# Kernel optimization log

Measured on AMD Instinct MI355X. Metric: run time of the kernel, lower is better.

## Reference

```python
import jax, jax.numpy as jnp
import numpy as np

B, N, D, L, H, DH, M, FF = 4, 2048, 512, 6, 8, 64, 266, 2048
EPS_LN = 1e-5
KERNEL_EPS = 1e-4


def fixed_pos_emb(n, dim):
    # performer_pytorch FixedPositionalEmbedding: cat(sin, cos) over half-dims
    inv_freq = 1.0 / (10000.0 ** (jnp.arange(0, dim, 2, dtype=jnp.float32) / dim))
    t = jnp.arange(n, dtype=jnp.float32)
    s = jnp.einsum('i,j->ij', t, inv_freq)  # [n, dim//2]
    return jnp.concatenate([jnp.sin(s), jnp.cos(s)], axis=-1)  # [n, dim]


def layer_norm(x, g, b):
    mu = x.mean(-1, keepdims=True)
    var = ((x - mu) ** 2).mean(-1, keepdims=True)
    return (x - mu) * jax.lax.rsqrt(var + EPS_LN) * g + b


def rotate_every_two(t):
    t1 = t[..., ::2]
    t2 = t[..., 1::2]
    return jnp.stack([-t2, t1], axis=-1).reshape(t.shape)


def apply_rotary(q, k, sinu):
    # sinu: [n, DH] = cat(sin_half, cos_half); repeat each value twice (interleaved)
    half = sinu.shape[-1] // 2
    sin = jnp.repeat(sinu[:, :half], 2, axis=-1)  # [n, DH]
    cos = jnp.repeat(sinu[:, half:], 2, axis=-1)
    q = q * cos + rotate_every_two(q) * sin
    k = k * cos + rotate_every_two(k) * sin
    return q, k


def softmax_kernel(data, proj, is_query):
    # data: [B,H,N,DH], proj: [M,DH]
    d = data.shape[-1]
    data_normalizer = d ** -0.25
    ratio = proj.shape[0] ** -0.5
    data_dash = jnp.einsum('bhnd,md->bhnm', data * data_normalizer, proj)
    diag = (data ** 2).sum(-1) * 0.5 * (data_normalizer ** 2)  # [B,H,N]
    if is_query:
        m = jnp.max(data_dash, axis=-1, keepdims=True)
    else:
        m = jnp.max(data_dash)
    return ratio * (jnp.exp(data_dash - diag[..., None] - m) + KERNEL_EPS)


def linear_attention(qf, kf, v):
    # qf/kf: [B,H,N,M], v: [B,H,N,DH]  (non-causal FAVOR+)
    k_sum = kf.sum(axis=-2)  # [B,H,M]
    d_inv = 1.0 / jnp.einsum('bhnm,bhm->bhn', qf, k_sum)
    context = jnp.einsum('bhnm,bhne->bhme', kf, v)  # [B,H,M,DH]
    return jnp.einsum('bhme,bhnm,bhn->bhne', context, qf, d_inv)


def setup_inputs() -> dict:
    key = jax.random.key(0)
    ks = jax.random.split(key, 8)
    std = 0.02
    inp = {
        'x': jax.random.normal(ks[0], (B, N, D), jnp.float32),
        'Wq': jax.random.normal(ks[1], (L, D, H * DH), jnp.float32) * std,
        'Wk': jax.random.normal(ks[2], (L, D, H * DH), jnp.float32) * std,
        'Wv': jax.random.normal(ks[3], (L, D, H * DH), jnp.float32) * std,
        'Wo': jax.random.normal(ks[4], (L, H * DH, D), jnp.float32) * std,
        'proj': jax.random.normal(ks[5], (L, M, DH), jnp.float32),
        'ln1_g': jnp.ones((L, D), jnp.float32),
        'ln1_b': jnp.zeros((L, D), jnp.float32),
        'W1': jax.random.normal(ks[6], (L, D, FF), jnp.float32) * std,
        'b1': jnp.zeros((L, FF), jnp.float32),
        'W2': jax.random.normal(ks[7], (L, FF, D), jnp.float32) * std,
        'b2': jnp.zeros((L, D), jnp.float32),
        'ln2_g': jnp.ones((L, D), jnp.float32),
        'ln2_b': jnp.zeros((L, D), jnp.float32),
        'lnf_g': jnp.ones((D,), jnp.float32),
        'lnf_b': jnp.zeros((D,), jnp.float32),
    }
    return inp


def reference(x, Wq, Wk, Wv, Wo, proj, ln1_g, ln1_b, W1, b1, W2, b2, ln2_g, ln2_b, lnf_g, lnf_b):
    n = x.shape[1]
    x = x + fixed_pos_emb(n, D)[None]          # additive sinusoidal emb
    sinu = fixed_pos_emb(n, DH)                 # per-head rotary table [n, DH]
    for i in range(L):
        # --- PreLayerNorm FAVOR+ self-attention ---
        h = layer_norm(x, ln1_g[i], ln1_b[i])
        q = jnp.einsum('bnd,de->bne', h, Wq[i]).reshape(B, n, H, DH).transpose(0, 2, 1, 3)
        k = jnp.einsum('bnd,de->bne', h, Wk[i]).reshape(B, n, H, DH).transpose(0, 2, 1, 3)
        v = jnp.einsum('bnd,de->bne', h, Wv[i]).reshape(B, n, H, DH).transpose(0, 2, 1, 3)
        q, k = apply_rotary(q, k, sinu)
        qf = softmax_kernel(q, proj[i], True)
        kf = softmax_kernel(k, proj[i], False)
        o = linear_attention(qf, kf, v)         # [B,H,n,DH]
        o = o.transpose(0, 2, 1, 3).reshape(B, n, H * DH)
        x = x + jnp.einsum('bne,ed->bnd', o, Wo[i])
        # --- PreLayerNorm FFN (GELU) ---
        h = layer_norm(x, ln2_g[i], ln2_b[i])
        h = jax.nn.gelu(jnp.einsum('bnd,df->bnf', h, W1[i]) + b1[i], approximate=False)
        x = x + jnp.einsum('bnf,fd->bnd', h, W2[i]) + b2[i]
    return layer_norm(x, lnf_g, lnf_b)
```

## Files before the change

### kernel.cpp

```cpp
#include <hip/hip_runtime.h>
#include <hip/hip_bf16.h>
#include <cstdint>

typedef float v4f __attribute__((ext_vector_type(4)));
typedef short v8s __attribute__((ext_vector_type(8)));
typedef unsigned short u16;

#define N_SEQ 2048
#define D_MODEL 512
#define N_LAYER 6
#define N_HEAD 8
#define D_HEAD 64
#define M_FEAT 266
#define M_PAD 288
#define M_ALLOC 384
#define FF_DIM 2048
#define BATCH 4
#define ROWS 8192
#define BHN 65536

__device__ __forceinline__ float b2f(u16 u) {
  return __uint_as_float(((uint32_t)u) << 16);
}
__device__ __forceinline__ u16 f2b(float f) {
  union { __hip_bfloat16 h; u16 u; } c;
  c.h = __float2bfloat16(f);
  return c.u;
}
__device__ __forceinline__ float wave_sum(float v) {
#pragma unroll
  for (int o = 1; o < 64; o <<= 1) v += __shfl_xor(v, o);
  return v;
}
__device__ __forceinline__ float wave_max(float v) {
#pragma unroll
  for (int o = 1; o < 64; o <<= 1) v = fmaxf(v, __shfl_xor(v, o));
  return v;
}

__device__ __forceinline__ float gelu_f(float x) {
  float ax = fabsf(x) * 0.70710678118f;
  float tt = __builtin_amdgcn_rcpf(fmaf(0.3275911f, ax, 1.0f));
  float poly = tt * fmaf(tt, fmaf(tt, fmaf(tt, fmaf(tt, 1.061405429f, -1.453152027f),
                                           1.421413741f), -0.284496736f), 0.254829592f);
  float er = 1.0f - poly * __expf(-ax * ax);
  er = copysignf(er, x);
  return 0.5f * x * (1.0f + er);
}

__device__ __forceinline__ void mfma_bf16(v4f& d, v8s a, v8s b) {
  asm volatile("v_mfma_f32_16x16x32_bf16 %0, %1, %2, %0" : "+v"(d) : "v"(a), "v"(b));
}

__device__ __forceinline__ void async16(const u16* g, u16* l) {
  __builtin_amdgcn_global_load_lds(
      (const __attribute__((address_space(1))) uint32_t*)g,
      (__attribute__((address_space(3))) uint32_t*)l, 16, 0, 0);
}

template <int EPI, int KSPLIT>
__global__ void __launch_bounds__(512, 4)
gemm4s(const u16* __restrict__ A, const u16* __restrict__ B,
       void* __restrict__ Cv, const float* __restrict__ bias,
       int K, int ldc)
{
  extern __shared__ u16 lds[];
  const int t = threadIdx.x;
  const int lane = t & 63;
  const int w = t >> 6;
  const int wm = w >> 2;
  const int wn = w & 3;
  const int tiM = blockIdx.x << 7, tiN = blockIdx.y << 8;
  const int ks = (KSPLIT > 1) ? blockIdx.z : 0;
  const int kchunk = K / KSPLIT;
  const int NT = kchunk >> 5;

  const int rr = lane & 15;
  const int kq = (lane >> 4) << 3;
  const int sw = ((rr >> 1) & 3) << 3;
  const int cr = kq ^ sw;

  const int srow = t >> 2;
  const int scol = (((t & 3) ^ ((srow >> 1) & 3)) << 3);
  const u16* Abase = A + (long long)(tiM + srow) * K + scol + (long long)ks * kchunk;
  const u16* Bbase = B + (long long)(tiN + srow) * K + scol + (long long)ks * kchunk;
  const long long r128 = 128LL * K;

  v4f acc[4][4] = {};

  auto stageA = [&](int s, int kt) {
    async16(Abase + (long long)kt * 32, &lds[s * 4096 + t * 8]);
  };
  auto stageB = [&](int s, int kt) {
    u16* d = &lds[16384 + s * 8192 + t * 8];
    async16(Bbase + (long long)kt * 32, d);
    async16(Bbase + (long long)kt * 32 + r128, d + 4096);
  };

  stageB(0, 0);
  stageA(0, 0);
  stageB(1, 1);
  stageA(1, 1);
  stageA(2, 2);
  asm volatile("s_waitcnt vmcnt(4)" ::: "memory");
  __builtin_amdgcn_s_barrier();

  for (int kt = 0; kt < NT; ++kt) {
    const int ab = (kt & 3) * 4096;
    const int bb = 16384 + (kt % 3) * 8192;
    if (kt + 2 < NT) stageB((kt + 2) % 3, kt + 2);
    if (kt + 3 < NT) stageA((kt + 3) & 3, kt + 3);
    v8s af[4], bf[4];
#pragma unroll
    for (int i = 0; i < 4; i++) {
      af[i] = *(const v8s*)&lds[ab + (wm * 64 + i * 16 + rr) * 32 + cr];
      bf[i] = *(const v8s*)&lds[bb + (wn * 64 + i * 16 + rr) * 32 + cr];
    }
    __builtin_amdgcn_s_setprio(1);
#pragma unroll
    for (int m = 0; m < 4; m++)
#pragma unroll
      for (int n = 0; n < 4; n++) mfma_bf16(acc[m][n], af[m], bf[n]);
    __builtin_amdgcn_s_setprio(0);
    if (kt + 1 < NT) {
      if (kt + 3 < NT)      asm volatile("s_waitcnt vmcnt(4)" ::: "memory");
      else if (kt + 2 < NT) asm volatile("s_waitcnt vmcnt(3)" ::: "memory");
      else                  asm volatile("s_waitcnt vmcnt(0)" ::: "memory");
      __builtin_amdgcn_s_barrier();
    }
  }

  __builtin_amdgcn_sched_barrier(0);
  asm volatile("s_nop 7\ns_nop 7\ns_nop 7");
  __builtin_amdgcn_sched_barrier(0);

  const int r4 = (lane >> 4) << 2;
  const int cc = lane & 15;
#pragma unroll
  for (int mf = 0; mf < 4; mf++)
#pragma unroll
    for (int nf = 0; nf < 4; nf++)
#pragma unroll
      for (int i = 0; i < 4; i++) {
        int row = tiM + wm * 64 + mf * 16 + r4 + i;
        int col = tiN + wn * 64 + nf * 16 + cc;
        float v = acc[mf][nf][i];
        if (EPI == 0) {
          ((u16*)Cv)[(long long)row * ldc + col] = f2b(v);
        } else if (EPI == 3) {
          ((u16*)Cv)[(long long)row * ldc + col] = f2b(gelu_f(v + bias[col]));
        } else {
          ((float*)Cv)[((long long)ks * ROWS + row) * ldc + col] = v;
        }
      }
}

template <bool LAST>
__global__ void ff2red_ln(const float* __restrict__ part, const float* __restrict__ bias,
                          float* __restrict__ x, const float* __restrict__ g,
                          const float* __restrict__ bvec, void* __restrict__ out)
{
  const int row = blockIdx.x * 4 + (threadIdx.x >> 6);
  const int lane = threadIdx.x & 63;
  const long long base = (long long)row * D_MODEL + lane * 8;
  v4f s0 = {}, s1 = {};
#pragma unroll
  for (int ks = 0; ks < 4; ks++) {
    const float* p = part + (long long)ks * (ROWS * 512LL) + base;
    s0 += *(const v4f*)p;
    s1 += *(const v4f*)(p + 4);
  }
  v4f b0 = *(const v4f*)(bias + lane * 8);
  v4f b1 = *(const v4f*)(bias + lane * 8 + 4);
  v4f x0 = *(const v4f*)(x + base) + s0 + b0;
  v4f x1 = *(const v4f*)(x + base + 4) + s1 + b1;
  if (!LAST) {
    *(v4f*)(x + base) = x0;
    *(v4f*)(x + base + 4) = x1;
  }
  float s = x0[0] + x0[1] + x0[2] + x0[3] + x1[0] + x1[1] + x1[2] + x1[3];
  float sq = x0[0]*x0[0] + x0[1]*x0[1] + x0[2]*x0[2] + x0[3]*x0[3]
           + x1[0]*x1[0] + x1[1]*x1[1] + x1[2]*x1[2] + x1[3]*x1[3];
  s = wave_sum(s);
  sq = wave_sum(sq);
  float mu = s * (1.0f / D_MODEL);
  float var = sq * (1.0f / D_MODEL) - mu * mu;
  float rstd = rsqrtf(var + 1e-5f);
  v4f g0 = *(const v4f*)(g + lane * 8), g1 = *(const v4f*)(g + lane * 8 + 4);
  v4f bb0 = *(const v4f*)(bvec + lane * 8), bb1 = *(const v4f*)(bvec + lane * 8 + 4);
  float y[8];
#pragma unroll
  for (int j = 0; j < 4; j++) y[j] = (x0[j] - mu) * rstd * g0[j] + bb0[j];
#pragma unroll
  for (int j = 0; j < 4; j++) y[4 + j] = (x1[j] - mu) * rstd * g1[j] + bb1[j];
  if (LAST) {
    float* op = (float*)out + base;
    v4f o0 = {y[0], y[1], y[2], y[3]}, o1 = {y[4], y[5], y[6], y[7]};
    *(v4f*)op = o0;
    *(v4f*)(op + 4) = o1;
  } else {
    u16* op = (u16*)out + base;
    alignas(16) u16 tmp[8];
#pragma unroll
    for (int j = 0; j < 8; j++) tmp[j] = f2b(y[j]);
    *(v8s*)op = *(v8s*)tmp;
  }
}

template <int EPI, int BN, int KSPLIT>
__global__ void __launch_bounds__(256, 4)
gemm2(const u16* __restrict__ A, const u16* __restrict__ B,
      void* __restrict__ Cv, const float* __restrict__ bias,
      int K, int ldc, long long sA, long long sB, long long sC,
      float scale, int Ncap, int Mcap, unsigned int* __restrict__ gmax)
{
  __shared__ u16 As[2][128 * 32];
  __shared__ u16 Bs[2][BN * 32];
  __shared__ float smax[4];
  const int zz = blockIdx.z;
  const int z = (KSPLIT > 1) ? zz / KSPLIT : zz;
  const int ks = (KSPLIT > 1) ? zz % KSPLIT : 0;
  const int kchunk = K / KSPLIT;
  const u16* Ag = A + (long long)z * sA + ks * kchunk;
  const u16* Bg = B + (long long)z * sB + ks * kchunk;
  const int t = threadIdx.x;
  const int lane = t & 63;
  const int w = t >> 6;
  constexpr int NF = BN / 32;
  const int wm = (w >> 1) << 6;
  const int wn = (w & 1) * (BN / 2);
  const int tiM = blockIdx.x << 7, tiN = blockIdx.y * BN;

  const int srow = t >> 2;
  const int scol = (t & 3) << 3;
  const u16* Ap = Ag + (long long)(tiM + srow) * K + scol;
  const u16* Bp = Bg + (long long)(tiN + srow) * K + scol;
  const long long rstride = 64LL * K;

  const int rr = lane & 15;
  const int kc = (lane >> 4) << 3;

  v4f acc[4][NF] = {};

  const int nk = kchunk >> 5;
  auto stage = [&](int buf, int k0) {
    async16(Ap + k0, &As[buf][t * 8]);
    async16(Ap + k0 + rstride, &As[buf][t * 8 + 2048]);
    async16(Bp + k0, &Bs[buf][t * 8]);
    if (BN == 128) async16(Bp + k0 + rstride, &Bs[buf][t * 8 + 2048]);
  };

  stage(0, 0);
  __syncthreads();
  int cur = 0;
  for (int kt = 0; kt < nk; ++kt) {
    if (kt + 1 < nk) stage(cur ^ 1, (kt + 1) << 5);
    v8s af[4], bf[NF];
#pragma unroll
    for (int i = 0; i < 4; i++) af[i] = *(const v8s*)&As[cur][(wm + rr + i * 16) * 32 + kc];
#pragma unroll
    for (int i = 0; i < NF; i++) bf[i] = *(const v8s*)&Bs[cur][(wn + rr + i * 16) * 32 + kc];
#pragma unroll
    for (int fm = 0; fm < 4; fm++)
#pragma unroll
      for (int fn = 0; fn < NF; fn++)
        mfma_bf16(acc[fm][fn], af[fm], bf[fn]);
    __syncthreads();
    cur ^= 1;
  }

  __builtin_amdgcn_sched_barrier(0);
  asm volatile("s_nop 7\ns_nop 7\ns_nop 7");
  __builtin_amdgcn_sched_barrier(0);

  const int r4 = (lane >> 4) << 2;
  const int cc = lane & 15;
  float lmax = -3e38f;
#pragma unroll
  for (int fm = 0; fm < 4; fm++)
#pragma unroll
    for (int fn = 0; fn < NF; fn++)
#pragma unroll
      for (int i = 0; i < 4; i++) {
        int row = tiM + wm + fm * 16 + r4 + i;
        int col = tiN + wn + fn * 16 + cc;
        float v = acc[fm][fn][i];
        if (EPI == 5) {
          if (row < Mcap && col < Ncap)
            ((float*)Cv)[((long long)zz * M_ALLOC + row) * 64 + col] = v;
        } else if (EPI == 7) {
          if (col < M_FEAT) lmax = fmaxf(lmax, v * scale);
        }
      }

  if (EPI == 7) {
    lmax = wave_max(lmax);
    if (lane == 0) smax[w] = lmax;
    __syncthreads();
    if (t == 0) {
      float m = fmaxf(fmaxf(smax[0], smax[1]), fmaxf(smax[2], smax[3]));
      unsigned int u = __float_as_uint(m);
      unsigned int key = (u & 0x80000000u) ? ~u : (u | 0x80000000u);
      atomicMax(gmax, key);
    }
  }
}

__global__ void __launch_bounds__(384, 3)
kf_gemm(const u16* __restrict__ kr, const u16* __restrict__ proj,
        const float* __restrict__ diagk, const unsigned int* __restrict__ kmax,
        u16* __restrict__ kfT, float* __restrict__ part)
{
  __shared__ u16 As[2][288 * 32];
  __shared__ u16 Bs[2][64 * 32];
  __shared__ float sdg[64];
  const int ntile = blockIdx.x;
  const int bh = blockIdx.z;
  const int n0 = ntile << 6;
  const int t = threadIdx.x;
  const int lane = t & 63;
  const int w = t >> 6;
  const u16* Bg = kr + (long long)bh * (N_SEQ * 64) + (long long)n0 * 64;
  const int rr = lane & 15, kc = (lane >> 4) << 3;

  if (t < 64) sdg[t] = diagk[(long long)bh * N_SEQ + n0 + t];
  unsigned int kk = kmax[0];
  const float km = (kk & 0x80000000u) ? __uint_as_float(kk ^ 0x80000000u)
                                      : __uint_as_float(~kk);

  v4f acc[3][4] = {};
  auto stage = [&](int buf, int k0) {
#pragma unroll
    for (int j = 0; j < 3; j++) {
      int idx = j * 384 + t;
      async16(proj + (long long)(idx >> 2) * 64 + ((idx & 3) << 3) + k0,
              &As[buf][j * 3072 + t * 8]);
    }
    if (t < 256) async16(Bg + (long long)(t >> 2) * 64 + ((t & 3) << 3) + k0,
                         &Bs[buf][t * 8]);
  };

  stage(0, 0);
  __syncthreads();
  for (int kt = 0; kt < 2; ++kt) {
    if (kt == 0) stage(1, 32);
    v8s af[3], bf[4];
#pragma unroll
    for (int i = 0; i < 3; i++) af[i] = *(const v8s*)&As[kt][(w * 48 + i * 16 + rr) * 32 + kc];
#pragma unroll
    for (int i = 0; i < 4; i++) bf[i] = *(const v8s*)&Bs[kt][(i * 16 + rr) * 32 + kc];
#pragma unroll
    for (int fm = 0; fm < 3; fm++)
#pragma unroll
      for (int fn = 0; fn < 4; fn++)
        mfma_bf16(acc[fm][fn], af[fm], bf[fn]);
    __syncthreads();
  }

  __builtin_amdgcn_sched_barrier(0);
  asm volatile("s_nop 7\ns_nop 7\ns_nop 7");
  __builtin_amdgcn_sched_barrier(0);

  const int r4 = (lane >> 4) << 2;
  const int cc = lane & 15;
  const float sc = 0.35355339f;

#pragma unroll
  for (int fm = 0; fm < 3; fm++)
#pragma unroll
    for (int i = 0; i < 4; i++) {
      int m = w * 48 + fm * 16 + r4 + i;
      float s = 0.0f;
#pragma unroll
      for (int fn = 0; fn < 4; fn++) {
        float dd = acc[fm][fn][i] * sc;
        float kf = (m < M_FEAT)
            ? 0.06131389f * (__expf(dd - sdg[fn * 16 + cc] - km) + 1e-4f) : 0.0f;
        acc[fm][fn][i] = kf;
        s += kf;
        kfT[((long long)bh * M_ALLOC + m) * N_SEQ + n0 + fn * 16 + cc] = f2b(kf);
      }
#pragma unroll
      for (int o = 1; o < 16; o <<= 1) s += __shfl_xor(s, o);
      if (cc == 0) part[((long long)bh * M_PAD + m) * 32 + ntile] = s;
    }
}

__global__ void ksumred(const float* __restrict__ part, float* __restrict__ ksum)
{
  int i = blockIdx.x * 256 + threadIdx.x;
  if (i >= 32 * M_PAD) return;
  const float* p = part + (long long)i * 32;
  float s = 0.0f;
#pragma unroll
  for (int j = 0; j < 32; j += 4) {
    v4f v = *(const v4f*)(p + j);
    s += v[0] + v[1] + v[2] + v[3];
  }
  ksum[i] = s;
}

template <int EPI>
__global__ void __launch_bounds__(256, 6)
gemm_small(const u16* __restrict__ A, const u16* __restrict__ B,
           void* __restrict__ Cv, const float* __restrict__ bias,
           int K, int ldc, long long sA, long long sB)
{
  __shared__ u16 As[2][64 * 32];
  __shared__ u16 Bs[2][64 * 32];
  const int z = blockIdx.z;
  const u16* Ag = A + (long long)z * sA;
  const u16* Bg = B + (long long)z * sB;
  const int t = threadIdx.x;
  const int lane = t & 63;
  const int w = t >> 6;
  const int wm = (w >> 1) << 5;
  const int wn = (w & 1) << 5;
  const int tiM = blockIdx.x << 6, tiN = blockIdx.y << 6;

  const int srow = t >> 2;
  const int scol = (t & 3) << 3;
  const u16* Ap = Ag + (long long)(tiM + srow) * K + scol;
  const u16* Bp = Bg + (long long)(tiN + srow) * K + scol;

  const int rr = lane & 15;
  const int kc = (lane >> 4) << 3;

  v4f acc[2][2] = {};

  const int nk = K >> 5;
  auto stage = [&](int buf, int k0) {
    async16(Ap + k0, &As[buf][t * 8]);
    async16(Bp + k0, &Bs[buf][t * 8]);
  };

  stage(0, 0);
  __syncthreads();
  int cur = 0;
  for (int kt = 0; kt < nk; ++kt) {
    if (kt + 1 < nk) stage(cur ^ 1, (kt + 1) << 5);
    v8s af[2], bf[2];
#pragma unroll
    for (int i = 0; i < 2; i++) af[i] = *(const v8s*)&As[cur][(wm + rr + i * 16) * 32 + kc];
#pragma unroll
    for (int i = 0; i < 2; i++) bf[i] = *(const v8s*)&Bs[cur][(wn + rr + i * 16) * 32 + kc];
#pragma unroll
    for (int fm = 0; fm < 2; fm++)
#pragma unroll
      for (int fn = 0; fn < 2; fn++)
        mfma_bf16(acc[fm][fn], af[fm], bf[fn]);
    __syncthreads();
    cur ^= 1;
  }

  __builtin_amdgcn_sched_barrier(0);
  asm volatile("s_nop 7\ns_nop 7\ns_nop 7");
  __builtin_amdgcn_sched_barrier(0);

  const int r4 = (lane >> 4) << 2;
  const int cc = lane & 15;
#pragma unroll
  for (int fm = 0; fm < 2; fm++)
#pragma unroll
    for (int fn = 0; fn < 2; fn++)
#pragma unroll
      for (int i = 0; i < 4; i++) {
        int row = tiM + wm + fm * 16 + r4 + i;
        int col = tiN + wn + fn * 16 + cc;
        float v = acc[fm][fn][i];
        if (EPI == 2) {
          long long idx = (long long)row * ldc + col;
          float bb = bias ? bias[col] : 0.0f;
          ((float*)Cv)[idx] += v + bb;
        } else {
          int b_ = z >> 3, h_ = z & 7;
          ((u16*)Cv)[(long long)(b_ * N_SEQ + row) * 512 + h_ * 64 + col] = f2b(v);
        }
      }
}

__global__ void __launch_bounds__(384, 3)
ddq_qf(const u16* __restrict__ qr, const u16* __restrict__ proj,
       const float* __restrict__ diag, const float* __restrict__ ksum,
       u16* __restrict__ qf)
{
  __shared__ u16 As[2][64 * 32];
  __shared__ u16 Bs[2][288 * 32];
  __shared__ float redw[6][64];
  __shared__ float rowv[64];
  __shared__ float sdg[64];
  const int bh = blockIdx.z;
  const int tiM = blockIdx.x << 6;
  const int t = threadIdx.x;
  const int lane = t & 63;
  const int w = t >> 6;
  const u16* Ag = qr + (long long)bh * (N_SEQ * 64);
  const int srow = t >> 2, scol = (t & 3) << 3;
  const u16* Ap = Ag + (long long)(tiM + srow) * 64 + scol;
  const int rr = lane & 15, kc = (lane >> 4) << 3;
  const int wn = w * 48;

  if (t < 64) sdg[t] = diag[(long long)bh * N_SEQ + tiM + t];

  v4f acc[4][3] = {};
  auto stage = [&](int buf, int k0) {
    if (t < 256) async16(Ap + k0, &As[buf][t * 8]);
#pragma unroll
    for (int j = 0; j < 3; j++) {
      int idx = j * 384 + t;
      async16(proj + (long long)(idx >> 2) * 64 + ((idx & 3) << 3) + k0,
              &Bs[buf][j * 3072 + t * 8]);
    }
  };

  stage(0, 0);
  __syncthreads();
  for (int kt = 0; kt < 2; ++kt) {
    if (kt == 0) stage(1, 32);
    v8s af[4], bf[3];
#pragma unroll
    for (int i = 0; i < 4; i++) af[i] = *(const v8s*)&As[kt][(rr + i * 16) * 32 + kc];
#pragma unroll
    for (int i = 0; i < 3; i++) bf[i] = *(const v8s*)&Bs[kt][(wn + i * 16 + rr) * 32 + kc];
#pragma unroll
    for (int fm = 0; fm < 4; fm++)
#pragma unroll
      for (int fn = 0; fn < 3; fn++)
        mfma_bf16(acc[fm][fn], af[fm], bf[fn]);
    __syncthreads();
  }

  __builtin_amdgcn_sched_barrier(0);
  asm volatile("s_nop 7\ns_nop 7\ns_nop 7");
  __builtin_amdgcn_sched_barrier(0);

  const int r4 = (lane >> 4) << 2;
  const int cc = lane & 15;
  const float sc = 0.35355339f;

#pragma unroll
  for (int fm = 0; fm < 4; fm++)
#pragma unroll
    for (int i = 0; i < 4; i++) {
      float m = -3e38f;
#pragma unroll
      for (int fn = 0; fn < 3; fn++) {
        int col = wn + fn * 16 + cc;
        float v = acc[fm][fn][i] * sc;
        if (col < M_FEAT) m = fmaxf(m, v);
      }
#pragma unroll
      for (int o = 1; o < 16; o <<= 1) m = fmaxf(m, __shfl_xor(m, o));
      if (cc == 0) redw[w][fm * 16 + r4 + i] = m;
    }
  __syncthreads();
  if (t < 64) {
    float g = redw[0][t];
#pragma unroll
    for (int ww = 1; ww < 6; ww++) g = fmaxf(g, redw[ww][t]);
    rowv[t] = g;
  }
  __syncthreads();

  float ksv[3];
#pragma unroll
  for (int fn = 0; fn < 3; fn++) ksv[fn] = ksum[bh * M_PAD + wn + fn * 16 + cc];

#pragma unroll
  for (int fm = 0; fm < 4; fm++)
#pragma unroll
    for (int i = 0; i < 4; i++) {
      int row = fm * 16 + r4 + i;
      float gm = rowv[row];
      float dg = sdg[row];
      float s = 0.0f;
#pragma unroll
      for (int fn = 0; fn < 3; fn++) {
        float e = 0.06131389f * (__expf(acc[fm][fn][i] * sc - dg - gm) + 1e-4f);
        acc[fm][fn][i] = e;
        s += e * ksv[fn];
      }
#pragma unroll
      for (int o = 1; o < 16; o <<= 1) s += __shfl_xor(s, o);
      if (cc == 0) redw[w][row] = s;
    }
  __syncthreads();
  if (t < 64) {
    float s = redw[0][t];
#pragma unroll
    for (int ww = 1; ww < 6; ww++) s += redw[ww][t];
    rowv[t] = 1.0f / s;
  }
  __syncthreads();

#pragma unroll
  for (int fm = 0; fm < 4; fm++)
#pragma unroll
    for (int i = 0; i < 4; i++) {
      int row = fm * 16 + r4 + i;
      float dinv = rowv[row];
#pragma unroll
      for (int fn = 0; fn < 3; fn++) {
        int col = wn + fn * 16 + cc;
        qf[((long long)bh * N_SEQ + tiM + row) * M_PAD + col] =
            f2b(acc[fm][fn][i] * dinv);
      }
    }
}

template <bool F32OUT>
__global__ void ln_kernel(const float* __restrict__ x, const float* __restrict__ g,
                          const float* __restrict__ b, void* __restrict__ out)
{
  const int row = blockIdx.x * 4 + (threadIdx.x >> 6);
  const int lane = threadIdx.x & 63;
  const float* xr = x + (long long)row * D_MODEL + lane * 8;
  v4f v0 = *(const v4f*)xr;
  v4f v1 = *(const v4f*)(xr + 4);
  float s = v0[0] + v0[1] + v0[2] + v0[3] + v1[0] + v1[1] + v1[2] + v1[3];
  float sq = v0[0]*v0[0] + v0[1]*v0[1] + v0[2]*v0[2] + v0[3]*v0[3]
           + v1[0]*v1[0] + v1[1]*v1[1] + v1[2]*v1[2] + v1[3]*v1[3];
  s = wave_sum(s);
  sq = wave_sum(sq);
  float mu = s * (1.0f / D_MODEL);
  float var = sq * (1.0f / D_MODEL) - mu * mu;
  float rstd = rsqrtf(var + 1e-5f);
  v4f g0 = *(const v4f*)(g + lane * 8), g1 = *(const v4f*)(g + lane * 8 + 4);
  v4f bb0 = *(const v4f*)(b + lane * 8), bb1 = *(const v4f*)(b + lane * 8 + 4);
  float y[8];
#pragma unroll
  for (int j = 0; j < 4; j++) y[j] = (v0[j] - mu) * rstd * g0[j] + bb0[j];
#pragma unroll
  for (int j = 0; j < 4; j++) y[4 + j] = (v1[j] - mu) * rstd * g1[j] + bb1[j];
  if (F32OUT) {
    float* op = (float*)out + (long long)row * D_MODEL + lane * 8;
    v4f o0 = {y[0], y[1], y[2], y[3]}, o1 = {y[4], y[5], y[6], y[7]};
    *(v4f*)op = o0;
    *(v4f*)(op + 4) = o1;
  } else {
    u16* op = (u16*)out + (long long)row * D_MODEL + lane * 8;
    alignas(16) u16 tmp[8];
#pragma unroll
    for (int j = 0; j < 8; j++) tmp[j] = f2b(y[j]);
    *(v8s*)op = *(v8s*)tmp;
  }
}

__global__ void posadd(const float* __restrict__ xin, float* __restrict__ x)
{
  long long i = (long long)blockIdx.x * 256 + threadIdx.x;
  int d = (int)(i & 511);
  int n = (int)((i >> 9) & 2047);
  int j = d & 255;
  float sarg = (float)n * expf(-0.035977892f * (float)j);
  float pe = (d < 256) ? sinf(sarg) : cosf(sarg);
  x[i] = xin[i] + pe;
}

__global__ void rotab(float* __restrict__ ts, float* __restrict__ tc)
{
  int i = blockIdx.x * 64 + threadIdx.x;
  int n = i >> 5, j = i & 31;
  float sarg = (float)n * expf(-0.28782314f * (float)j);
  float s, c;
  sincosf(sarg, &s, &c);
  ts[i] = s;
  tc[i] = c;
}

__global__ void __launch_bounds__(256)
rotvt(const u16* __restrict__ qkv,
      const float* __restrict__ ts, const float* __restrict__ tc,
      u16* __restrict__ qr, u16* __restrict__ kr, u16* __restrict__ vT,
      float* __restrict__ dq, float* __restrict__ dk)
{
  __shared__ u16 st[64][72];
  const int bid = blockIdx.x;
  const int nt = bid & 31;
  const int h = (bid >> 5) & 7;
  const int b = bid >> 8;
  const int t = threadIdx.x;
  const int r = t >> 3;
  const int cg = t & 7;
#pragma unroll
  for (int it = 0; it < 2; ++it) {
    const int nl = it * 32 + r;
    const int n = nt * 64 + nl;
    const long long src = ((long long)(b * N_SEQ + n)) * 1536 + h * 64 + cg * 8;
    v8s q8 = *(const v8s*)(qkv + src);
    v8s k8 = *(const v8s*)(qkv + src + 512);
    v8s v8 = *(const v8s*)(qkv + src + 1024);
    v4f sn = *(const v4f*)(ts + n * 32 + cg * 4);
    v4f cn = *(const v4f*)(tc + n * 32 + cg * 4);
    alignas(16) u16 qo[8], ko[8];
    float q2 = 0.0f, k2 = 0.0f;
#pragma unroll
    for (int j = 0; j < 4; j++) {
      float qe = b2f((u16)q8[2 * j]), qoe = b2f((u16)q8[2 * j + 1]);
      float ke = b2f((u16)k8[2 * j]), koe = b2f((u16)k8[2 * j + 1]);
      float c = cn[j], s = sn[j];
      float q0 = qe * c - qoe * s, q1 = qoe * c + qe * s;
      float k0 = ke * c - koe * s, k1 = koe * c + ke * s;
      qo[2 * j] = f2b(q0); qo[2 * j + 1] = f2b(q1);
      ko[2 * j] = f2b(k0); ko[2 * j + 1] = f2b(k1);
      q2 += q0 * q0 + q1 * q1;
      k2 += k0 * k0 + k1 * k1;
    }
    q2 += __shfl_xor(q2, 1); q2 += __shfl_xor(q2, 2); q2 += __shfl_xor(q2, 4);
    k2 += __shfl_xor(k2, 1); k2 += __shfl_xor(k2, 2); k2 += __shfl_xor(k2, 4);
    const long long rowidx = (long long)(b * 8 + h) * N_SEQ + n;
    if (cg == 0) {
      dq[rowidx] = q2 * 0.0625f;
      dk[rowidx] = k2 * 0.0625f;
    }
    *(v8s*)(qr + rowidx * 64 + cg * 8) = *(v8s*)qo;
    *(v8s*)(kr + rowidx * 64 + cg * 8) = *(v8s*)ko;
    *(v8s*)&st[nl][cg * 8] = v8;
  }
  __syncthreads();
  const int r2 = t >> 2, c2 = (t & 3) << 4;
  alignas(16) u16 tmp[16];
#pragma unroll
  for (int jj = 0; jj < 16; jj++) tmp[jj] = st[c2 + jj][r2];
  const long long dst = ((long long)((b * 8 + h) * 64 + r2)) * N_SEQ + nt * 64 + c2;
  *(v8s*)(vT + dst) = *(v8s*)&tmp[0];
  *(v8s*)(vT + dst + 8) = *(v8s*)&tmp[8];
}

__global__ void wtrans(const float* __restrict__ src, u16* __restrict__ dst,
                       int Ks, int Ns, long long sSrc, long long sDst)
{
  int l = blockIdx.z;
  src += (long long)l * sSrc;
  dst += (long long)l * sDst;
  int n0 = blockIdx.x << 6, k0 = blockIdx.y << 6;
  __shared__ float st[64][68];
  int t = threadIdx.x;
  int r = t >> 2, c = (t & 3) << 4;
  const float* sp = src + (long long)(k0 + r) * Ns + n0 + c;
#pragma unroll
  for (int jj = 0; jj < 16; jj += 4) *(v4f*)&st[r][c + jj] = *(const v4f*)(sp + jj);
  __syncthreads();
  alignas(16) u16 tmp[16];
#pragma unroll
  for (int jj = 0; jj < 16; jj++) tmp[jj] = f2b(st[c + jj][r]);
  u16* dp = dst + (long long)(n0 + r) * Ks + k0 + c;
  *(v8s*)(dp) = *(v8s*)&tmp[0];
  *(v8s*)(dp + 8) = *(v8s*)&tmp[8];
}

__global__ void projconv(const float* __restrict__ proj, u16* __restrict__ out)
{
  int i = blockIdx.x * 256 + threadIdx.x;
  int dh = i & 63;
  int m = (i >> 6) % M_ALLOC;
  int l = i / (M_ALLOC * 64);
  float v = (m < M_FEAT) ? proj[((long long)l * M_FEAT + m) * 64 + dh] : 0.0f;
  out[i] = f2b(v);
}

__global__ void resetmax(unsigned int* p) { *p = 0u; }

__global__ void ctxred(const float* __restrict__ part, u16* __restrict__ ctxT)
{
  int bh = blockIdx.y;
  int m0 = blockIdx.x << 6;
  __shared__ float st[64][65];
  int t = threadIdx.x;
  int r = t >> 2, c = (t & 3) << 4;
  int m = m0 + r;
  v4f s[4] = {};
  if (m < M_PAD) {
    for (int ks = 0; ks < 8; ks++) {
      const float* p = part + (((long long)bh * 8 + ks) * M_ALLOC + m) * 64 + c;
#pragma unroll
      for (int j = 0; j < 4; j++) s[j] += *(const v4f*)(p + j * 4);
    }
  }
#pragma unroll
  for (int j = 0; j < 4; j++)
#pragma unroll
    for (int e = 0; e < 4; e++) st[r][c + j * 4 + e] = s[j][e];
  __syncthreads();
  int e = t >> 2, mc = (t & 3) << 4;
  if (m0 + mc < M_PAD) {
    alignas(16) u16 tmp[16];
#pragma unroll
    for (int j = 0; j < 16; j++) tmp[j] = f2b(st[mc + j][e]);
    u16* op = ctxT + ((long long)bh * 64 + e) * M_PAD + m0 + mc;
    *(v8s*)op = *(v8s*)&tmp[0];
    *(v8s*)(op + 8) = *(v8s*)&tmp[8];
  }
}

extern "C" void kernel_launch(void* const* d_in, const int* in_sizes, int n_in,
                              void* d_out, int out_size, void* d_ws, size_t ws_size,
                              hipStream_t stream)
{
  const float* x_in = (const float*)d_in[0];
  const float* Wq  = (const float*)d_in[1];
  const float* Wk  = (const float*)d_in[2];
  const float* Wv  = (const float*)d_in[3];
  const float* Wo  = (const float*)d_in[4];
  const float* Pr  = (const float*)d_in[5];
  const float* ln1g = (const float*)d_in[6];
  const float* ln1b = (const float*)d_in[7];
  const float* W1  = (const float*)d_in[8];
  const float* b1  = (const float*)d_in[9];
  const float* W2  = (const float*)d_in[10];
  const float* b2  = (const float*)d_in[11];
  const float* ln2g = (const float*)d_in[12];
  const float* ln2b = (const float*)d_in[13];
  const float* lnfg = (const float*)d_in[14];
  const float* lnfb = (const float*)d_in[15];

  hipFuncSetAttribute(reinterpret_cast<const void*>(&gemm4s<0, 1>),
                      hipFuncAttributeMaxDynamicSharedMemorySize, 81920);
  hipFuncSetAttribute(reinterpret_cast<const void*>(&gemm4s<3, 1>),
                      hipFuncAttributeMaxDynamicSharedMemorySize, 81920);
  hipFuncSetAttribute(reinterpret_cast<const void*>(&gemm4s<5, 4>),
                      hipFuncAttributeMaxDynamicSharedMemorySize, 81920);

  char* ws = (char*)d_ws;
  size_t off = 0;
  auto alloc = [&](size_t bytes) -> void* {
    void* p = ws + off;
    off = (off + bytes + 255) & ~(size_t)255;
    return p;
  };

  float* x      = (float*)alloc((size_t)ROWS * D_MODEL * 4);
  float* tsin   = (float*)alloc((size_t)N_SEQ * 32 * 4);
  float* tcos   = (float*)alloc((size_t)N_SEQ * 32 * 4);
  u16*   wqkvT  = (u16*)alloc((size_t)N_LAYER * 1536 * 512 * 2);
  u16*   woT    = (u16*)alloc((size_t)N_LAYER * 512 * 512 * 2);
  u16*   w1T    = (u16*)alloc((size_t)N_LAYER * 2048 * 512 * 2);
  u16*   w2T    = (u16*)alloc((size_t)N_LAYER * 512 * 2048 * 2);
  u16*   projT  = (u16*)alloc((size_t)N_LAYER * M_ALLOC * 64 * 2);
  u16*   hbuf   = (u16*)alloc((size_t)ROWS * D_MODEL * 2);
  u16*   obuf   = (u16*)alloc((size_t)ROWS * D_MODEL * 2);
  float* big    = (float*)alloc((size_t)32 * N_SEQ * M_PAD * 4);
  u16*   qrbuf  = (u16*)alloc((size_t)BHN * 64 * 2);
  u16*   krbuf  = (u16*)alloc((size_t)BHN * 64 * 2);
  u16*   vTbuf  = (u16*)alloc((size_t)BHN * 64 * 2);
  float* diagq  = (float*)alloc((size_t)BHN * 4);
  float* diagk  = (float*)alloc((size_t)BHN * 4);
  unsigned int* kmaxu = (unsigned int*)alloc(256);
  u16*   kfT    = (u16*)alloc((size_t)32 * M_ALLOC * N_SEQ * 2);
  float* part   = (float*)alloc((size_t)32 * 8 * M_ALLOC * 64 * 4);
  float* kspart = (float*)alloc((size_t)32 * M_PAD * 32 * 4);
  u16*   ctxT   = (u16*)alloc((size_t)32 * 64 * M_PAD * 2);
  float* ksum   = (float*)alloc((size_t)32 * M_PAD * 4);
  (void)alloc(1 << 20);
  (void)ws_size; (void)in_sizes; (void)n_in; (void)out_size;
  float* ff2part = (float*)kfT;

  posadd<<<16384, 256, 0, stream>>>(x_in, x);
  rotab<<<1024, 64, 0, stream>>>(tsin, tcos);
  wtrans<<<dim3(8, 8, 6), 256, 0, stream>>>(Wq, wqkvT, 512, 512, 512LL * 512, 1536LL * 512);
  wtrans<<<dim3(8, 8, 6), 256, 0, stream>>>(Wk, wqkvT + 512LL * 512, 512, 512, 512LL * 512, 1536LL * 512);
  wtrans<<<dim3(8, 8, 6), 256, 0, stream>>>(Wv, wqkvT + 1024LL * 512, 512, 512, 512LL * 512, 1536LL * 512);
  wtrans<<<dim3(8, 8, 6), 256, 0, stream>>>(Wo, woT, 512, 512, 512LL * 512, 512LL * 512);
  wtrans<<<dim3(32, 8, 6), 256, 0, stream>>>(W1, w1T, 512, 2048, 512LL * 2048, 2048LL * 512);
  wtrans<<<dim3(8, 32, 6), 256, 0, stream>>>(W2, w2T, 2048, 512, 2048LL * 512, 512LL * 2048);
  projconv<<<(N_LAYER * M_ALLOC * 64) / 256, 256, 0, stream>>>(Pr, projT);

  ln_kernel<false><<<ROWS / 4, 256, 0, stream>>>(x, ln1g, ln1b, hbuf);

  for (int l = 0; l < N_LAYER; l++) {
    const u16* wq = wqkvT + (long long)l * 1536 * 512;
    const u16* wo = woT + (long long)l * 512 * 512;
    const u16* w1 = w1T + (long long)l * 2048 * 512;
    const u16* w2 = w2T + (long long)l * 512 * 2048;
    const u16* pj = projT + (long long)l * M_ALLOC * 64;

    resetmax<<<1, 1, 0, stream>>>(kmaxu);
    gemm4s<0, 1><<<dim3(64, 6), 512, 81920, stream>>>(hbuf, wq, big, nullptr, 512, 1536);
    rotvt<<<1024, 256, 0, stream>>>((u16*)big, tsin, tcos, qrbuf, krbuf, vTbuf, diagq, diagk);
    gemm2<7, 128, 1><<<dim3(512, 3, 1), 256, 0, stream>>>(krbuf, pj, nullptr, nullptr,
        64, M_PAD, 0, 0, 0, 0.35355339f, M_PAD, BHN, kmaxu);
    kf_gemm<<<dim3(32, 1, 32), 384, 0, stream>>>(krbuf, pj, diagk, kmaxu, kfT, kspart);
    ksumred<<<(32 * M_PAD + 255) / 256, 256, 0, stream>>>(kspart, ksum);
    gemm2<5, 64, 8><<<dim3(3, 1, 256), 256, 0, stream>>>(kfT, vTbuf, part, nullptr,
        2048, 64, (long long)M_ALLOC * N_SEQ, 64LL * N_SEQ, 0, 1.0f, 64, M_PAD, nullptr);
    ctxred<<<dim3(5, 32), 256, 0, stream>>>(part, ctxT);
    ddq_qf<<<dim3(32, 1, 32), 384, 0, stream>>>(qrbuf, pj, diagq, ksum, kfT);
    gemm_small<4><<<dim3(32, 1, 32), 256, 0, stream>>>(kfT, ctxT, obuf, nullptr,
        M_PAD, 0, (long long)N_SEQ * M_PAD, 64LL * M_PAD);
    gemm_small<2><<<dim3(128, 8, 1), 256, 0, stream>>>(obuf, wo, x, nullptr,
        512, 512, 0, 0);
    ln_kernel<false><<<ROWS / 4, 256, 0, stream>>>(x, ln2g + l * 512, ln2b + l * 512, hbuf);
    gemm4s<3, 1><<<dim3(64, 8), 512, 81920, stream>>>(hbuf, w1, big, b1 + (long long)l * 2048,
        512, 2048);
    gemm4s<5, 4><<<dim3(64, 2, 4), 512, 81920, stream>>>((u16*)big, w2, ff2part, nullptr,
        2048, 512);
    if (l < N_LAYER - 1) {
      ff2red_ln<false><<<2048, 256, 0, stream>>>(ff2part, b2 + (long long)l * 512, x,
          ln1g + (long long)(l + 1) * 512, ln1b + (long long)(l + 1) * 512, hbuf);
    } else {
      ff2red_ln<true><<<2048, 256, 0, stream>>>(ff2part, b2 + (long long)l * 512, x,
          lnfg, lnfb, d_out);
    }
  }
}
```

Baseline: 1.406 ms.

## Fuse query feature map with context GEMM to produce attention output directly

The qf kernel now keeps the normalized query features in shared memory and multiplies them by the per-head context matrix in the same block. The output rows go straight to obuf, so the separate gemm_small<4> launch is gone, along with the round trip of the full qf tensor through global memory. The cost is 75 KB of dynamic LDS per block, which may lower occupancy, and only 4 of the 6 waves do the second GEMM. Unused template branches in gemm_small and ln_kernel are removed as cleanup.

```diff
diff --git a/kernel.cpp b/kernel.cpp
--- a/kernel.cpp
+++ b/kernel.cpp
@@ -468,24 +468,18 @@
         int row = tiM + wm + fm * 16 + r4 + i;
         int col = tiN + wn + fn * 16 + cc;
         float v = acc[fm][fn][i];
-        if (EPI == 2) {
-          long long idx = (long long)row * ldc + col;
-          float bb = bias ? bias[col] : 0.0f;
-          ((float*)Cv)[idx] += v + bb;
-        } else {
-          int b_ = z >> 3, h_ = z & 7;
-          ((u16*)Cv)[(long long)(b_ * N_SEQ + row) * 512 + h_ * 64 + col] = f2b(v);
-        }
+        long long idx = (long long)row * ldc + col;
+        float bb = bias ? bias[col] : 0.0f;
+        ((float*)Cv)[idx] += v + bb;
       }
 }
 
 __global__ void __launch_bounds__(384, 3)
-ddq_qf(const u16* __restrict__ qr, const u16* __restrict__ proj,
-       const float* __restrict__ diag, const float* __restrict__ ksum,
-       u16* __restrict__ qf)
-{
-  __shared__ u16 As[2][64 * 32];
-  __shared__ u16 Bs[2][288 * 32];
+ddq_qf_o(const u16* __restrict__ qr, const u16* __restrict__ proj,
+         const float* __restrict__ diag, const float* __restrict__ ksum,
+         const u16* __restrict__ ctxT, u16* __restrict__ obuf)
+{
+  extern __shared__ u16 dl[];
   __shared__ float redw[6][64];
   __shared__ float rowv[64];
   __shared__ float sdg[64];
@@ -495,8 +489,7 @@
   const int lane = t & 63;
   const int w = t >> 6;
   const u16* Ag = qr + (long long)bh * (N_SEQ * 64);
-  const int srow = t >> 2, scol = (t & 3) << 3;
-  const u16* Ap = Ag + (long long)(tiM + srow) * 64 + scol;
+  const u16* Ap = Ag + (long long)(tiM + (t >> 2)) * 64 + ((t & 3) << 3);
   const int rr = lane & 15, kc = (lane >> 4) << 3;
   const int wn = w * 48;
 
@@ -504,12 +497,12 @@
 
   v4f acc[4][3] = {};
   auto stage = [&](int buf, int k0) {
-    if (t < 256) async16(Ap + k0, &As[buf][t * 8]);
+    if (t < 256) async16(Ap + k0, &dl[buf * 2048 + t * 8]);
 #pragma unroll
     for (int j = 0; j < 3; j++) {
       int idx = j * 384 + t;
       async16(proj + (long long)(idx >> 2) * 64 + ((idx & 3) << 3) + k0,
-              &Bs[buf][j * 3072 + t * 8]);
+              &dl[4096 + buf * 9216 + j * 3072 + t * 8]);
     }
   };
 
@@ -519,9 +512,11 @@
     if (kt == 0) stage(1, 32);
     v8s af[4], bf[3];
 #pragma unroll
-    for (int i = 0; i < 4; i++) af[i] = *(const v8s*)&As[kt][(rr + i * 16) * 32 + kc];
-#pragma unroll
-    for (int i = 0; i < 3; i++) bf[i] = *(const v8s*)&Bs[kt][(wn + i * 16 + rr) * 32 + kc];
+    for (int i = 0; i < 4; i++)
+      af[i] = *(const v8s*)&dl[kt * 2048 + (rr + i * 16) * 32 + kc];
+#pragma unroll
+    for (int i = 0; i < 3; i++)
+      bf[i] = *(const v8s*)&dl[4096 + kt * 9216 + (wn + i * 16 + rr) * 32 + kc];
 #pragma unroll
     for (int fm = 0; fm < 4; fm++)
 #pragma unroll
@@ -533,6 +528,14 @@
   __builtin_amdgcn_sched_barrier(0);
   asm volatile("s_nop 7\ns_nop 7\ns_nop 7");
   __builtin_amdgcn_sched_barrier(0);
+
+  v8s creg[6];
+  const u16* cb = ctxT + (long long)bh * (64 * M_PAD);
+#pragma unroll
+  for (int j = 0; j < 6; j++) {
+    int slot = j * 384 + t;
+    creg[j] = *(const v8s*)(cb + (slot / 36) * M_PAD + (slot % 36) * 8);
+  }
 
   const int r4 = (lane >> 4) << 2;
   const int cc = lane & 15;
@@ -600,15 +603,41 @@
       int row = fm * 16 + r4 + i;
       float dinv = rowv[row];
 #pragma unroll
-      for (int fn = 0; fn < 3; fn++) {
-        int col = wn + fn * 16 + cc;
-        qf[((long long)bh * N_SEQ + tiM + row) * M_PAD + col] =
-            f2b(acc[fm][fn][i] * dinv);
+      for (int fn = 0; fn < 3; fn++)
+        dl[row * 296 + wn + fn * 16 + cc] = f2b(acc[fm][fn][i] * dinv);
+    }
+#pragma unroll
+  for (int j = 0; j < 6; j++) {
+    int slot = j * 384 + t;
+    *(v8s*)&dl[18944 + (slot / 36) * 296 + (slot % 36) * 8] = creg[j];
+  }
+  __syncthreads();
+
+  if (w < 4) {
+    v4f oacc[4] = {};
+    for (int kk = 0; kk < 9; kk++) {
+      v8s aq = *(const v8s*)&dl[(w * 16 + rr) * 296 + kk * 32 + kc];
+#pragma unroll
+      for (int et = 0; et < 4; et++) {
+        v8s bc = *(const v8s*)&dl[18944 + (et * 16 + rr) * 296 + kk * 32 + kc];
+        mfma_bf16(oacc[et], aq, bc);
       }
     }
-}
-
-template <bool F32OUT>
+    __builtin_amdgcn_sched_barrier(0);
+    asm volatile("s_nop 7\ns_nop 7\ns_nop 7");
+    __builtin_amdgcn_sched_barrier(0);
+    const int b_ = bh >> 3, h_ = bh & 7;
+#pragma unroll
+    for (int et = 0; et < 4; et++)
+#pragma unroll
+      for (int i = 0; i < 4; i++) {
+        int n = tiM + w * 16 + r4 + i;
+        obuf[((long long)(b_ * N_SEQ + n)) * 512 + h_ * 64 + et * 16 + cc] =
+            f2b(oacc[et][i]);
+      }
+  }
+}
+
 __global__ void ln_kernel(const float* __restrict__ x, const float* __restrict__ g,
                           const float* __restrict__ b, void* __restrict__ out)
 {
@@ -632,18 +661,11 @@
   for (int j = 0; j < 4; j++) y[j] = (v0[j] - mu) * rstd * g0[j] + bb0[j];
 #pragma unroll
   for (int j = 0; j < 4; j++) y[4 + j] = (v1[j] - mu) * rstd * g1[j] + bb1[j];
-  if (F32OUT) {
-    float* op = (float*)out + (long long)row * D_MODEL + lane * 8;
-    v4f o0 = {y[0], y[1], y[2], y[3]}, o1 = {y[4], y[5], y[6], y[7]};
-    *(v4f*)op = o0;
-    *(v4f*)(op + 4) = o1;
-  } else {
-    u16* op = (u16*)out + (long long)row * D_MODEL + lane * 8;
-    alignas(16) u16 tmp[8];
-#pragma unroll
-    for (int j = 0; j < 8; j++) tmp[j] = f2b(y[j]);
-    *(v8s*)op = *(v8s*)tmp;
-  }
+  u16* op = (u16*)out + (long long)row * D_MODEL + lane * 8;
+  alignas(16) u16 tmp[8];
+#pragma unroll
+  for (int j = 0; j < 8; j++) tmp[j] = f2b(y[j]);
+  *(v8s*)op = *(v8s*)tmp;
 }
 
 __global__ void posadd(const float* __restrict__ xin, float* __restrict__ x)
@@ -820,6 +842,8 @@
                       hipFuncAttributeMaxDynamicSharedMemorySize, 81920);
   hipFuncSetAttribute(reinterpret_cast<const void*>(&gemm4s<5, 4>),
                       hipFuncAttributeMaxDynamicSharedMemorySize, 81920);
+  hipFuncSetAttribute(reinterpret_cast<const void*>(&ddq_qf_o),
+                      hipFuncAttributeMaxDynamicSharedMemorySize, 75776);
 
   char* ws = (char*)d_ws;
   size_t off = 0;
@@ -865,7 +889,7 @@
   wtrans<<<dim3(8, 32, 6), 256, 0, stream>>>(W2, w2T, 2048, 512, 2048LL * 512, 512LL * 2048);
   projconv<<<(N_LAYER * M_ALLOC * 64) / 256, 256, 0, stream>>>(Pr, projT);
 
-  ln_kernel<false><<<ROWS / 4, 256, 0, stream>>>(x, ln1g, ln1b, hbuf);
+  ln_kernel<<<ROWS / 4, 256, 0, stream>>>(x, ln1g, ln1b, hbuf);
 
   for (int l = 0; l < N_LAYER; l++) {
     const u16* wq = wqkvT + (long long)l * 1536 * 512;
@@ -884,12 +908,10 @@
     gemm2<5, 64, 8><<<dim3(3, 1, 256), 256, 0, stream>>>(kfT, vTbuf, part, nullptr,
         2048, 64, (long long)M_ALLOC * N_SEQ, 64LL * N_SEQ, 0, 1.0f, 64, M_PAD, nullptr);
     ctxred<<<dim3(5, 32), 256, 0, stream>>>(part, ctxT);
-    ddq_qf<<<dim3(32, 1, 32), 384, 0, stream>>>(qrbuf, pj, diagq, ksum, kfT);
-    gemm_small<4><<<dim3(32, 1, 32), 256, 0, stream>>>(kfT, ctxT, obuf, nullptr,
-        M_PAD, 0, (long long)N_SEQ * M_PAD, 64LL * M_PAD);
+    ddq_qf_o<<<dim3(32, 1, 32), 384, 75776, stream>>>(qrbuf, pj, diagq, ksum, ctxT, obuf);
     gemm_small<2><<<dim3(128, 8, 1), 256, 0, stream>>>(obuf, wo, x, nullptr,
         512, 512, 0, 0);
-    ln_kernel<false><<<ROWS / 4, 256, 0, stream>>>(x, ln2g + l * 512, ln2b + l * 512, hbuf);
+    ln_kernel<<<ROWS / 4, 256, 0, stream>>>(x, ln2g + l * 512, ln2b + l * 512, hbuf);
     gemm4s<3, 1><<<dim3(64, 8), 512, 81920, stream>>>(hbuf, w1, big, b1 + (long long)l * 2048,
         512, 2048);
     gemm4s<5, 4><<<dim3(64, 2, 4), 512, 81920, stream>>>((u16*)big, w2, ff2part, nullptr,
```

Measured after the change: 1.392 ms. No clear change (-1.0%).
